# Performance work log

Hardware: AMD Instinct MI355X
Metric: run time of the kernel (lower is better)

Reference implementation:

```python
import jax, jax.numpy as jnp
import numpy as np

RMAX = 5.0   # max_radius
NB = 8       # bessel bases
NSH = 9      # (lmax+1)^2, lmax=2
S = 4        # message passing steps


def _rms(x):
    return x * jax.lax.rsqrt(jnp.mean(x * x, axis=-1, keepdims=True) + 1e-6)


def _mlp(x, w1, b1, w2, b2):
    # 2-layer MLP (base_mlp_depth=2) with silu activation + rms_norm output
    return _rms(jax.nn.silu(x @ w1 + b1) @ w2 + b2)


def _sh(u):
    # real spherical harmonics up to l=2, component normalization (e3nn style), u: [E,3] unit vectors
    x, y, z = u[:, 0], u[:, 1], u[:, 2]
    s3, s5, s15 = 3.0 ** 0.5, 5.0 ** 0.5, 15.0 ** 0.5
    return jnp.stack([
        jnp.ones_like(x),
        s3 * x, s3 * y, s3 * z,
        s15 * x * y, s15 * y * z, 0.5 * s5 * (3.0 * z * z - 1.0),
        s15 * x * z, 0.5 * s15 * (x * x - y * y)], axis=1)


def setup_inputs() -> dict:
    key = jax.random.key(0)
    ks = iter(jax.random.split(key, 64))
    N, E, D, H, L, BOND = 20000, 640000, 128, 256, 128, 16

    def w(shape, fan):
        return jax.random.normal(next(ks), shape, jnp.float32) / np.float32(np.sqrt(fan))

    return dict(
        pos=jax.random.normal(next(ks), (N, 3), jnp.float32),
        c_in=jnp.ones((1,), jnp.float32),
        atom_type_index=jax.random.randint(next(ks), (N,), 0, 20),
        atom_code_index=jax.random.randint(next(ks), (N,), 0, 10),
        residue_code_index=jax.random.randint(next(ks), (N,), 0, 25),
        residue_sequence_index=jnp.zeros((N,), jnp.int32),  # max_sequence_length=1
        senders=jax.random.randint(next(ks), (E,), 0, N),
        receivers=jax.random.randint(next(ks), (E,), 0, N),
        bond_mask=jax.random.randint(next(ks), (E,), 0, 2),
        emb_at=w((20, 32), 1.0), emb_ac=w((10, 32), 1.0),
        emb_rc=w((25, 32), 1.0), emb_ri=w((1, 32), 1.0),
        emb_bond=w((2, BOND), 1.0),
        nenc_w1=w((D, H), D), nenc_b1=jnp.zeros((H,), jnp.float32),
        nenc_w2=w((H, L), H), nenc_b2=jnp.zeros((L,), jnp.float32),
        eenc_w1=w((NB * NSH + BOND, H), NB * NSH + BOND), eenc_b1=jnp.zeros((H,), jnp.float32),
        eenc_w2=w((H, L), H), eenc_b2=jnp.zeros((L,), jnp.float32),
        msg_w1=w((S, 3 * L, H), 3 * L), msg_b1=jnp.zeros((S, H), jnp.float32),
        msg_w2=w((S, H, L), H), msg_b2=jnp.zeros((S, L), jnp.float32),
        gate_w=w((S, L, 1), L), gate_b=jnp.zeros((S, 1), jnp.float32),
        upd_w1=w((S, 2 * L, H), 2 * L), upd_b1=jnp.zeros((S, H), jnp.float32),
        upd_w2=w((S, H, L), H), upd_b2=jnp.zeros((S, L), jnp.float32),
        head_w1=w((L, H), L), head_b1=jnp.zeros((H,), jnp.float32),
        head_w2=w((H, 3), H), head_b2=jnp.zeros((3,), jnp.float32),
    )


def reference(pos, c_in, atom_type_index, atom_code_index, residue_code_index,
              residue_sequence_index, senders, receivers, bond_mask,
              emb_at, emb_ac, emb_rc, emb_ri, emb_bond,
              nenc_w1, nenc_b1, nenc_w2, nenc_b2,
              eenc_w1, eenc_b1, eenc_w2, eenc_b2,
              msg_w1, msg_b1, msg_w2, msg_b2, gate_w, gate_b,
              upd_w1, upd_b1, upd_w2, upd_b2,
              head_w1, head_b1, head_w2, head_b2):
    N = pos.shape[0]
    E = senders.shape[0]

    # --- update_features: embeddings + edge vectors ---
    node_emb = jnp.concatenate([
        emb_at[atom_type_index], emb_ac[atom_code_index],
        emb_rc[residue_code_index], emb_ri[residue_sequence_index]], axis=1)  # [N,128]
    bond_emb = emb_bond[bond_mask]                                            # [E,16]

    up = pos / c_in
    vec = up[senders] - up[receivers]                                         # [E,3]
    r = jnp.sqrt(jnp.sum(vec * vec, axis=-1) + 1e-12)                         # [E]
    u = vec / r[:, None]

    # Bessel RBF: sqrt(2/rmax) * sin(n*pi*r/rmax) / r
    n = jnp.arange(1, NB + 1, dtype=jnp.float32)
    rbf = jnp.sqrt(2.0 / RMAX) * jnp.sin(n[None, :] * jnp.pi * r[:, None] / RMAX) / r[:, None]
    # cosine distance cutoff envelope
    cut = 0.5 * (jnp.cos(jnp.pi * jnp.minimum(r, RMAX) / RMAX) + 1.0) * (r < RMAX)

    ylm = _sh(u)                                                              # [E,9]
    radial = (rbf[:, :, None] * ylm[:, None, :]).reshape(E, NB * NSH) * cut[:, None]

    # --- encoders ---
    h = _mlp(node_emb, nenc_w1, nenc_b1, nenc_w2, nenc_b2)                    # [N,L]
    e = _mlp(jnp.concatenate([radial, bond_emb], axis=1),
             eenc_w1, eenc_b1, eenc_w2, eenc_b2)                              # [E,L]

    # --- message passing: gather -> MLP -> sigmoid-gate * cutoff -> scatter ---
    for s in range(S):
        m = _mlp(jnp.concatenate([h[senders], h[receivers], e], axis=1),
                 msg_w1[s], msg_b1[s], msg_w2[s], msg_b2[s])                  # [E,L]
        g = jax.nn.sigmoid(m @ gate_w[s] + gate_b[s]) * cut[:, None]          # [E,1]
        agg = jax.ops.segment_sum(m * g, receivers, num_segments=N)           # [N,L]
        h = h + _mlp(jnp.concatenate([h, agg], axis=1),
                     upd_w1[s], upd_b1[s], upd_w2[s], upd_b2[s])
        e = e + m

    # --- head: predict per-node 3-vector ---
    return jax.nn.silu(h @ head_w1 + head_b1) @ head_w2 + head_b2             # [N,3]
```

## Files before the change

kernel.cpp:

```cpp
#include <hip/hip_runtime.h>
#include <hip/hip_bf16.h>
#include <math.h>


#define TILE   16
#define STRIDE 20

using short8 = __attribute__((ext_vector_type(8))) short;
using f32x4  = __attribute__((ext_vector_type(4))) float;

__device__ __forceinline__ float silu_f(float x) {
  return x / (1.0f + __expf(-x));
}
__device__ __forceinline__ unsigned short f2b(float x) {
  union { __hip_bfloat16 b; unsigned short u; } v;
  v.b = __float2bfloat16(x);
  return v.u;
}
__device__ __forceinline__ float b2f(unsigned short h) {
  union { unsigned u; float f; } v; v.u = ((unsigned)h) << 16;
  return v.f;
}

__global__ __launch_bounds__(256) void pack_w_kernel(
    const float* __restrict__ src, unsigned short* __restrict__ dst,
    int Kreal, int KS, int NF)
{
  const int N = NF * 16;
  const int total = NF * KS * 512;
  for (int idx = blockIdx.x * 256 + threadIdx.x; idx < total; idx += gridDim.x * 256) {
    const int nf  = idx / (KS * 512);
    const int rem = idx - nf * (KS * 512);
    const int kk  = rem >> 9;
    const int p   = rem & 511;
    const int l   = p >> 3, j = p & 7;
    const int c   = nf * 16 + (l & 15);
    const int k   = kk * 32 + ((l >> 4) << 3) + j;
    dst[idx] = (k < Kreal) ? f2b(src[(size_t)k * N + c]) : (unsigned short)0;
  }
}

template<int KS1>
__device__ __forceinline__ void mfma_l1_compute(const unsigned short* __restrict__ x1,
                                                const unsigned short* __restrict__ w1p,
                                                int tid, f32x4 acc[8])
{
  const int w  = tid >> 6;
  const int l  = tid & 63;
  const int lr = l & 15;
  const int lk = (l >> 4) << 3;
  const int RS = KS1 * 32;
  const f32x4 zz = {0.f, 0.f, 0.f, 0.f};
  #pragma unroll
  for (int i = 0; i < 8; ++i) acc[i] = zz;

  for (int kk = 0; kk < KS1; ++kk) {
    short8 af[2];
    #pragma unroll
    for (int mf = 0; mf < 2; ++mf) {
      const int r = mf * 16 + lr;
      const int k = kk * 32 + lk;
      af[mf] = *(const short8*)&x1[r * RS + ((((k >> 3) ^ (r & 7))) << 3)];
    }
    #pragma unroll
    for (int nf = 0; nf < 4; ++nf) {
      const int nfg = w * 4 + nf;
      const short8 bf = *(const short8*)&w1p[(size_t)(((nfg * KS1) + kk) * 64 + l) * 8];
      #pragma unroll
      for (int mf = 0; mf < 2; ++mf)
        acc[mf * 4 + nf] = __builtin_amdgcn_mfma_f32_16x16x32_bf16(af[mf], bf, acc[mf * 4 + nf], 0, 0, 0);
    }
  }
}

__device__ __forceinline__ void l1_store_silu(const f32x4 acc[8],
                                              const float* __restrict__ b1,
                                              unsigned short* __restrict__ hsm,
                                              int tid)
{
  const int w = tid >> 6, l = tid & 63, lr = l & 15;
  #pragma unroll
  for (int nf = 0; nf < 4; ++nf) {
    const int c = (w * 4 + nf) * 16 + lr;
    const float bias = b1[c];
    #pragma unroll
    for (int mf = 0; mf < 2; ++mf) {
      #pragma unroll
      for (int q = 0; q < 4; ++q) {
        const int r = mf * 16 + ((l >> 4) << 2) + q;
        const float v = silu_f(acc[mf * 4 + nf][q] + bias);
        hsm[r * 256 + (((c >> 3) ^ (r & 7)) << 3) + (c & 7)] = f2b(v);
      }
    }
  }
}

__device__ __forceinline__ void mfma_l2(const unsigned short* __restrict__ hsm,
                                        const unsigned short* __restrict__ w2p,
                                        const float* __restrict__ b2,
                                        int tid, f32x4 acc2[4])
{
  const int w  = tid >> 6;
  const int l  = tid & 63;
  const int lr = l & 15;
  const int lk = (l >> 4) << 3;
  const f32x4 zz = {0.f, 0.f, 0.f, 0.f};
  #pragma unroll
  for (int i = 0; i < 4; ++i) acc2[i] = zz;

  for (int kk = 0; kk < 8; ++kk) {
    short8 af[2];
    #pragma unroll
    for (int mf = 0; mf < 2; ++mf) {
      const int r = mf * 16 + lr;
      const int k = kk * 32 + lk;
      af[mf] = *(const short8*)&hsm[r * 256 + (((k >> 3) ^ (r & 7)) << 3)];
    }
    #pragma unroll
    for (int nf2 = 0; nf2 < 2; ++nf2) {
      const int nfg = w * 2 + nf2;
      const short8 bf = *(const short8*)&w2p[(size_t)(((nfg * 8) + kk) * 64 + l) * 8];
      #pragma unroll
      for (int mf = 0; mf < 2; ++mf)
        acc2[mf * 2 + nf2] = __builtin_amdgcn_mfma_f32_16x16x32_bf16(af[mf], bf, acc2[mf * 2 + nf2], 0, 0, 0);
    }
  }
  #pragma unroll
  for (int nf2 = 0; nf2 < 2; ++nf2) {
    const float bias = b2[(w * 2 + nf2) * 16 + lr];
    #pragma unroll
    for (int mf = 0; mf < 2; ++mf) {
      #pragma unroll
      for (int q = 0; q < 4; ++q) acc2[mf * 2 + nf2][q] += bias;
    }
  }
}

__device__ __forceinline__ void rms_reduce(const f32x4 acc2[4], float* rsum,
                                           int tid, float mval[2][2][4])
{
  const int l = tid & 63;
  #pragma unroll
  for (int mf = 0; mf < 2; ++mf) {
    #pragma unroll
    for (int q = 0; q < 4; ++q) {
      float s = acc2[mf * 2][q] * acc2[mf * 2][q]
              + acc2[mf * 2 + 1][q] * acc2[mf * 2 + 1][q];
      s += __shfl_xor(s, 1); s += __shfl_xor(s, 2);
      s += __shfl_xor(s, 4); s += __shfl_xor(s, 8);
      if ((l & 15) == 0)
        atomicAdd(&rsum[mf * 16 + ((l >> 4) << 2) + q], s);
    }
  }
  __syncthreads();
  #pragma unroll
  for (int mf = 0; mf < 2; ++mf) {
    #pragma unroll
    for (int q = 0; q < 4; ++q) {
      const int r = mf * 16 + ((l >> 4) << 2) + q;
      const float inv = rsqrtf(rsum[r] * (1.0f / 128.0f) + 1e-6f);
      #pragma unroll
      for (int nf2 = 0; nf2 < 2; ++nf2)
        mval[mf][nf2][q] = acc2[mf * 2 + nf2][q] * inv;
    }
  }
}

__global__ __launch_bounds__(256, 5) void edge_enc_mfma(
    const float* __restrict__ pos, const float* __restrict__ c_in,
    const int* __restrict__ snd, const int* __restrict__ rcv,
    const int* __restrict__ bnd, const float* __restrict__ embb,
    const unsigned short* __restrict__ w1p, const float* __restrict__ b1,
    const unsigned short* __restrict__ w2p, const float* __restrict__ b2,
    unsigned short* __restrict__ e_g, float* __restrict__ cutb, int E)
{
  __shared__ __align__(16) unsigned short smem[32 * 256];
  unsigned short* x1  = smem;
  unsigned short* hsm = smem;
  __shared__ float grbf[32][8];
  __shared__ float gylm[32][9];
  __shared__ float gcut[32];
  __shared__ int   gbond[32];
  __shared__ float rsum[32];
  const int tid = threadIdx.x;
  const int e0  = blockIdx.x * 32;

  if (tid < 32) {
    rsum[tid] = 0.f;
    const int ed = min(e0 + tid, E - 1);
    const int sa = snd[ed], ra = rcv[ed];
    const float ci = c_in[0];
    const float vx = (pos[sa * 3 + 0] - pos[ra * 3 + 0]) / ci;
    const float vy = (pos[sa * 3 + 1] - pos[ra * 3 + 1]) / ci;
    const float vz = (pos[sa * 3 + 2] - pos[ra * 3 + 2]) / ci;
    const float r  = sqrtf(vx * vx + vy * vy + vz * vz + 1e-12f);
    const float ir = 1.0f / r;
    const float ux = vx * ir, uy = vy * ir, uz = vz * ir;
    const float PI = 3.14159265358979323846f;
    const float pr = PI * r * 0.2f;
    const float c0 = 0.632455532033675866f;
    #pragma unroll
    for (int n = 0; n < 8; ++n)
      grbf[tid][n] = c0 * sinf((float)(n + 1) * pr) * ir;
    const float cv = 0.5f * (cosf(PI * fminf(r, 5.0f) * 0.2f) + 1.0f)
                   * (r < 5.0f ? 1.0f : 0.0f);
    gcut[tid] = cv;
    if (e0 + tid < E) cutb[e0 + tid] = cv;
    const float s3  = 1.7320508075688772f;
    const float s5  = 2.2360679774997896f;
    const float s15 = 3.8729833462074170f;
    gylm[tid][0] = 1.0f;
    gylm[tid][1] = s3 * ux; gylm[tid][2] = s3 * uy; gylm[tid][3] = s3 * uz;
    gylm[tid][4] = s15 * ux * uy; gylm[tid][5] = s15 * uy * uz;
    gylm[tid][6] = 0.5f * s5 * (3.0f * uz * uz - 1.0f);
    gylm[tid][7] = s15 * ux * uz;
    gylm[tid][8] = 0.5f * s15 * (ux * ux - uy * uy);
    gbond[tid] = bnd[ed];
  }
  __syncthreads();
  for (int i = tid; i < 32 * 16; i += 256) {
    const int r = i >> 4, g = i & 15;
    union { short8 v; unsigned short u[8]; } t;
    #pragma unroll
    for (int j = 0; j < 8; ++j) {
      const int k = g * 8 + j;
      float v;
      if (k < 72) { const int n = k / 9, mm = k - 9 * n; v = grbf[r][n] * gylm[r][mm] * gcut[r]; }
      else if (k < 88) v = embb[gbond[r] * 16 + (k - 72)];
      else v = 0.f;
      t.u[j] = f2b(v);
    }
    *(short8*)&x1[r * 128 + ((g ^ (r & 7)) << 3)] = t.v;
  }
  __syncthreads();
  f32x4 acc1[8];
  mfma_l1_compute<4>(x1, w1p, tid, acc1);
  __syncthreads();
  l1_store_silu(acc1, b1, hsm, tid);
  __syncthreads();
  f32x4 acc2[4];
  mfma_l2(hsm, w2p, b2, tid, acc2);
  float mval[2][2][4];
  rms_reduce(acc2, rsum, tid, mval);
  const int l = tid & 63, w = tid >> 6, lr = l & 15;
  #pragma unroll
  for (int mf = 0; mf < 2; ++mf) {
    #pragma unroll
    for (int q = 0; q < 4; ++q) {
      const int r = mf * 16 + ((l >> 4) << 2) + q;
      const int ed = e0 + r;
      if (ed < E) {
        #pragma unroll
        for (int nf2 = 0; nf2 < 2; ++nf2) {
          const int c2 = (w * 2 + nf2) * 16 + lr;
          e_g[(size_t)ed * 128 + c2] = f2b(mval[mf][nf2][q]);
        }
      }
    }
  }
}

__global__ __launch_bounds__(256, 5) void msg_mfma(
    const unsigned short* __restrict__ hb, unsigned short* __restrict__ e_g,
    float* __restrict__ agg, const float* __restrict__ cutb,
    const int* __restrict__ snd, const int* __restrict__ rcv,
    const unsigned short* __restrict__ w1p, const float* __restrict__ b1,
    const unsigned short* __restrict__ w2p, const float* __restrict__ b2,
    const float* __restrict__ gw, const float* __restrict__ gb, int E)
{
  __shared__ __align__(16) unsigned short smem[32 * 384];
  unsigned short* x1  = smem;
  unsigned short* hsm = smem;
  __shared__ int   snd_s[32], rcv_s[32];
  __shared__ float cut_s[32];
  __shared__ float rsum[32], gsum[32];
  const int tid = threadIdx.x;
  const int e0  = blockIdx.x * 32;

  if (tid < 32) {
    rsum[tid] = 0.f; gsum[tid] = 0.f;
    const int ed = min(e0 + tid, E - 1);
    snd_s[tid] = snd[ed]; rcv_s[tid] = rcv[ed]; cut_s[tid] = cutb[ed];
  }
  __syncthreads();
  for (int i = tid; i < 32 * 48; i += 256) {
    const int r = i / 48, g = i - r * 48;
    short8 t;
    if (g < 32) {
      const int node = (g < 16) ? snd_s[r] : rcv_s[r];
      t = *(const short8*)&hb[(size_t)node * 128 + (g & 15) * 8];
    } else {
      const int ed = min(e0 + r, E - 1);
      t = *(const short8*)&e_g[(size_t)ed * 128 + (g - 32) * 8];
    }
    *(short8*)&x1[r * 384 + ((g ^ (r & 7)) << 3)] = t;
  }
  __syncthreads();
  f32x4 acc1[8];
  mfma_l1_compute<12>(x1, w1p, tid, acc1);

  const int l = tid & 63, w = tid >> 6, lr = l & 15;
  float eold[16];
  {
    int idx = 0;
    #pragma unroll
    for (int mf = 0; mf < 2; ++mf) {
      #pragma unroll
      for (int q = 0; q < 4; ++q) {
        const int r = mf * 16 + ((l >> 4) << 2) + q;
        #pragma unroll
        for (int nf2 = 0; nf2 < 2; ++nf2) {
          const int k = 256 + (w * 2 + nf2) * 16 + lr;
          eold[idx++] = b2f(x1[r * 384 + (((k >> 3) ^ (r & 7)) << 3) + (k & 7)]);
        }
      }
    }
  }
  __syncthreads();
  l1_store_silu(acc1, b1, hsm, tid);
  __syncthreads();
  f32x4 acc2[4];
  mfma_l2(hsm, w2p, b2, tid, acc2);
  float mval[2][2][4];
  rms_reduce(acc2, rsum, tid, mval);

  const float gw0 = gw[(w * 2 + 0) * 16 + lr];
  const float gw1 = gw[(w * 2 + 1) * 16 + lr];
  #pragma unroll
  for (int mf = 0; mf < 2; ++mf) {
    #pragma unroll
    for (int q = 0; q < 4; ++q) {
      float p = mval[mf][0][q] * gw0 + mval[mf][1][q] * gw1;
      p += __shfl_xor(p, 1); p += __shfl_xor(p, 2);
      p += __shfl_xor(p, 4); p += __shfl_xor(p, 8);
      if ((l & 15) == 0)
        atomicAdd(&gsum[mf * 16 + ((l >> 4) << 2) + q], p);
    }
  }
  __syncthreads();
  const float gbv = gb[0];
  {
    int idx = 0;
    #pragma unroll
    for (int mf = 0; mf < 2; ++mf) {
      #pragma unroll
      for (int q = 0; q < 4; ++q) {
        const int r = mf * 16 + ((l >> 4) << 2) + q;
        const int ed = e0 + r;
        if (ed < E) {
          const float gr = cut_s[r] / (1.0f + __expf(-(gsum[r] + gbv)));
          const int rv = rcv_s[r];
          #pragma unroll
          for (int nf2 = 0; nf2 < 2; ++nf2) {
            const int c2 = (w * 2 + nf2) * 16 + lr;
            const float m = mval[mf][nf2][q];
            e_g[(size_t)ed * 128 + c2] = f2b(eold[idx] + m);
            atomicAdd(&agg[(size_t)rv * 128 + c2], m * gr);
            ++idx;
          }
        } else {
          idx += 2;
        }
      }
    }
  }
}

__global__ __launch_bounds__(256, 5) void upd_mfma(
    float* __restrict__ h, unsigned short* __restrict__ hb,
    float* __restrict__ agg,
    const unsigned short* __restrict__ w1p, const float* __restrict__ b1,
    const unsigned short* __restrict__ w2p, const float* __restrict__ b2,
    int N)
{
  __shared__ __align__(16) unsigned short smem[32 * 256];
  unsigned short* x1  = smem;
  unsigned short* hsm = smem;
  __shared__ float rsum[32];
  const int tid = threadIdx.x;
  const int n0  = blockIdx.x * 32;
  if (tid < 32) rsum[tid] = 0.f;
  __syncthreads();
  for (int i = tid; i < 32 * 32; i += 256) {
    const int r = i >> 5, g = i & 31;
    const int n = min(n0 + r, N - 1);
    short8 t;
    if (g < 16) {
      t = *(const short8*)&hb[(size_t)n * 128 + g * 8];
    } else {
      const float4 f0 = *(const float4*)&agg[(size_t)n * 128 + (g - 16) * 8];
      const float4 f1 = *(const float4*)&agg[(size_t)n * 128 + (g - 16) * 8 + 4];
      union { short8 v; unsigned short u[8]; } tt;
      tt.u[0] = f2b(f0.x); tt.u[1] = f2b(f0.y); tt.u[2] = f2b(f0.z); tt.u[3] = f2b(f0.w);
      tt.u[4] = f2b(f1.x); tt.u[5] = f2b(f1.y); tt.u[6] = f2b(f1.z); tt.u[7] = f2b(f1.w);
      t = tt.v;
    }
    *(short8*)&x1[r * 256 + ((g ^ (r & 7)) << 3)] = t;
  }
  __syncthreads();
  for (int i = tid; i < 1024; i += 256) {
    const int r = i >> 5, c4 = i & 31;
    const int n = n0 + r;
    if (n < N) *(float4*)&agg[(size_t)n * 128 + c4 * 4] = make_float4(0.f, 0.f, 0.f, 0.f);
  }
  f32x4 acc1[8];
  mfma_l1_compute<8>(x1, w1p, tid, acc1);
  __syncthreads();
  l1_store_silu(acc1, b1, hsm, tid);
  __syncthreads();
  f32x4 acc2[4];
  mfma_l2(hsm, w2p, b2, tid, acc2);
  float mval[2][2][4];
  rms_reduce(acc2, rsum, tid, mval);
  const int l = tid & 63, w = tid >> 6, lr = l & 15;
  #pragma unroll
  for (int mf = 0; mf < 2; ++mf) {
    #pragma unroll
    for (int q = 0; q < 4; ++q) {
      const int r = mf * 16 + ((l >> 4) << 2) + q;
      const int n = n0 + r;
      if (n < N) {
        #pragma unroll
        for (int nf2 = 0; nf2 < 2; ++nf2) {
          const int c2 = (w * 2 + nf2) * 16 + lr;
          const float nh = h[(size_t)n * 128 + c2] + mval[mf][nf2][q];
          h[(size_t)n * 128 + c2]  = nh;
          hb[(size_t)n * 128 + c2] = f2b(nh);
        }
      }
    }
  }
}


__device__ __forceinline__ float loadE(const float* p)          { return *p; }
__device__ __forceinline__ float loadE(const __hip_bfloat16* p) { return __bfloat162float(*p); }
__device__ __forceinline__ void  storeE(float* p, float v)          { *p = v; }
__device__ __forceinline__ void  storeE(__hip_bfloat16* p, float v) { *p = __float2bfloat16(v); }

template<int K1>
__device__ __forceinline__ void layer1_silu(const float* __restrict__ xs,
                                            const float* __restrict__ w1,
                                            const float* __restrict__ b1,
                                            float* __restrict__ hs, int tid)
{
  const int jh = tid & 127;
  const int tp = tid >> 7;
  const int tbase = 8 * tp;
  float a[8] = {0,0,0,0,0,0,0,0};
  float b[8] = {0,0,0,0,0,0,0,0};
  const float* wp = w1 + jh;
  for (int k = 0; k < K1; ++k) {
    const float4 x0 = *(const float4*)&xs[k*STRIDE + tbase];
    const float4 x1 = *(const float4*)&xs[k*STRIDE + tbase + 4];
    const float wa = wp[k*256];
    const float wb = wp[k*256 + 128];
    a[0] = fmaf(x0.x, wa, a[0]); a[1] = fmaf(x0.y, wa, a[1]);
    a[2] = fmaf(x0.z, wa, a[2]); a[3] = fmaf(x0.w, wa, a[3]);
    a[4] = fmaf(x1.x, wa, a[4]); a[5] = fmaf(x1.y, wa, a[5]);
    a[6] = fmaf(x1.z, wa, a[6]); a[7] = fmaf(x1.w, wa, a[7]);
    b[0] = fmaf(x0.x, wb, b[0]); b[1] = fmaf(x0.y, wb, b[1]);
    b[2] = fmaf(x0.z, wb, b[2]); b[3] = fmaf(x0.w, wb, b[3]);
    b[4] = fmaf(x1.x, wb, b[4]); b[5] = fmaf(x1.y, wb, b[5]);
    b[6] = fmaf(x1.z, wb, b[6]); b[7] = fmaf(x1.w, wb, b[7]);
  }
  const float ba = b1[jh];
  const float bb = b1[jh + 128];
  float4 oa0, oa1, ob0, ob1;
  oa0.x = silu_f(a[0] + ba); oa0.y = silu_f(a[1] + ba);
  oa0.z = silu_f(a[2] + ba); oa0.w = silu_f(a[3] + ba);
  oa1.x = silu_f(a[4] + ba); oa1.y = silu_f(a[5] + ba);
  oa1.z = silu_f(a[6] + ba); oa1.w = silu_f(a[7] + ba);
  ob0.x = silu_f(b[0] + bb); ob0.y = silu_f(b[1] + bb);
  ob0.z = silu_f(b[2] + bb); ob0.w = silu_f(b[3] + bb);
  ob1.x = silu_f(b[4] + bb); ob1.y = silu_f(b[5] + bb);
  ob1.z = silu_f(b[6] + bb); ob1.w = silu_f(b[7] + bb);
  *(float4*)&hs[jh*STRIDE + tbase]           = oa0;
  *(float4*)&hs[jh*STRIDE + tbase + 4]       = oa1;
  *(float4*)&hs[(jh+128)*STRIDE + tbase]     = ob0;
  *(float4*)&hs[(jh+128)*STRIDE + tbase + 4] = ob1;
}

__device__ __forceinline__ void layer2_bias(const float* __restrict__ hs,
                                            const float* __restrict__ w2,
                                            const float* __restrict__ b2,
                                            int tid, float cA[4], float cB[4])
{
  const int dh = tid & 63;
  const int tq = tid >> 6;
  const int tbase = 4 * tq;
  cA[0]=cA[1]=cA[2]=cA[3]=0.0f;
  cB[0]=cB[1]=cB[2]=cB[3]=0.0f;
  const float* wp = w2 + dh;
  for (int k = 0; k < 256; ++k) {
    const float4 hv = *(const float4*)&hs[k*STRIDE + tbase];
    const float wa = wp[k*128];
    const float wb = wp[k*128 + 64];
    cA[0] = fmaf(hv.x, wa, cA[0]); cA[1] = fmaf(hv.y, wa, cA[1]);
    cA[2] = fmaf(hv.z, wa, cA[2]); cA[3] = fmaf(hv.w, wa, cA[3]);
    cB[0] = fmaf(hv.x, wb, cB[0]); cB[1] = fmaf(hv.y, wb, cB[1]);
    cB[2] = fmaf(hv.z, wb, cB[2]); cB[3] = fmaf(hv.w, wb, cB[3]);
  }
  const float b2a = b2[dh];
  const float b2b = b2[dh + 64];
  #pragma unroll
  for (int tt = 0; tt < 4; ++tt) { cA[tt] += b2a; cB[tt] += b2b; }
}

__device__ __forceinline__ void rms4(float cA[4], float cB[4])
{
  float s[4];
  #pragma unroll
  for (int tt = 0; tt < 4; ++tt) s[tt] = cA[tt]*cA[tt] + cB[tt]*cB[tt];
  #pragma unroll
  for (int off = 32; off; off >>= 1) {
    #pragma unroll
    for (int tt = 0; tt < 4; ++tt) s[tt] += __shfl_xor(s[tt], off);
  }
  #pragma unroll
  for (int tt = 0; tt < 4; ++tt) {
    const float inv = rsqrtf(s[tt] * (1.0f/128.0f) + 1e-6f);
    cA[tt] *= inv; cB[tt] *= inv;
  }
}

__global__ __launch_bounds__(256) void zero_kernel(float4* __restrict__ p, int n4)
{
  const int i = blockIdx.x * 256 + threadIdx.x;
  if (i < n4) p[i] = make_float4(0.f, 0.f, 0.f, 0.f);
}

__global__ __launch_bounds__(256) void node_enc_kernel(
    const int* __restrict__ ati, const int* __restrict__ aci,
    const int* __restrict__ rci, const int* __restrict__ rsi,
    const float* __restrict__ emb_at, const float* __restrict__ emb_ac,
    const float* __restrict__ emb_rc, const float* __restrict__ emb_ri,
    const float* __restrict__ w1, const float* __restrict__ b1,
    const float* __restrict__ w2, const float* __restrict__ b2,
    float* __restrict__ h, unsigned short* __restrict__ hb, int N)
{
  __shared__ __align__(16) float xs[128*STRIDE];
  __shared__ __align__(16) float hs[256*STRIDE];
  __shared__ int idx_s[4][TILE];
  const int tid = threadIdx.x;
  const int n0 = blockIdx.x * TILE;
  if (tid < TILE) {
    const int n = min(n0 + tid, N - 1);
    idx_s[0][tid] = ati[n]; idx_s[1][tid] = aci[n];
    idx_s[2][tid] = rci[n]; idx_s[3][tid] = rsi[n];
  }
  __syncthreads();
  for (int i = tid; i < TILE*128; i += 256) {
    const int t = i >> 7, k = i & 127;
    const int seg = k >> 5, kk = k & 31;
    const float* tab = (seg == 0) ? emb_at : (seg == 1) ? emb_ac
                     : (seg == 2) ? emb_rc : emb_ri;
    xs[k*STRIDE + t] = tab[idx_s[seg][t]*32 + kk];
  }
  __syncthreads();
  layer1_silu<128>(xs, w1, b1, hs, tid);
  __syncthreads();
  float cA[4], cB[4];
  layer2_bias(hs, w2, b2, tid, cA, cB);
  rms4(cA, cB);
  const int dh = tid & 63, tq = tid >> 6;
  #pragma unroll
  for (int tt = 0; tt < 4; ++tt) {
    const int n = n0 + 4*tq + tt;
    if (n < N) {
      h[(size_t)n*128 + dh]      = cA[tt];
      h[(size_t)n*128 + dh + 64] = cB[tt];
      if (hb) {
        hb[(size_t)n*128 + dh]      = f2b(cA[tt]);
        hb[(size_t)n*128 + dh + 64] = f2b(cB[tt]);
      }
    }
  }
}

template<typename ET>
__global__ __launch_bounds__(256) void edge_enc_kernel(
    const float* __restrict__ pos, const float* __restrict__ c_in,
    const int* __restrict__ snd, const int* __restrict__ rcv,
    const int* __restrict__ bnd, const float* __restrict__ emb_bond,
    const float* __restrict__ w1, const float* __restrict__ b1,
    const float* __restrict__ w2, const float* __restrict__ b2,
    ET* __restrict__ e, float* __restrict__ cutb, int E)
{
  __shared__ __align__(16) float xs[88*STRIDE];
  __shared__ __align__(16) float hs[256*STRIDE];
  __shared__ float grbf[TILE][8];
  __shared__ float gylm[TILE][9];
  __shared__ float gcut[TILE];
  __shared__ int   gbond[TILE];
  const int tid = threadIdx.x;
  const int e0 = blockIdx.x * TILE;
  if (tid < TILE) {
    const int ed = min(e0 + tid, E - 1);
    const int sa = snd[ed], ra = rcv[ed];
    const float ci = c_in[0];
    const float vx = (pos[sa*3+0] - pos[ra*3+0]) / ci;
    const float vy = (pos[sa*3+1] - pos[ra*3+1]) / ci;
    const float vz = (pos[sa*3+2] - pos[ra*3+2]) / ci;
    const float r  = sqrtf(vx*vx + vy*vy + vz*vz + 1e-12f);
    const float ir = 1.0f / r;
    const float ux = vx*ir, uy = vy*ir, uz = vz*ir;
    const float PI = 3.14159265358979323846f;
    const float pr = PI * r * 0.2f;
    const float c0 = 0.632455532033675866f;
    #pragma unroll
    for (int n = 0; n < 8; ++n)
      grbf[tid][n] = c0 * sinf((float)(n + 1) * pr) * ir;
    const float cv = 0.5f * (cosf(PI * fminf(r, 5.0f) * 0.2f) + 1.0f)
                   * (r < 5.0f ? 1.0f : 0.0f);
    gcut[tid] = cv;
    cutb[ed] = cv;
    const float s3  = 1.7320508075688772f;
    const float s5  = 2.2360679774997896f;
    const float s15 = 3.8729833462074170f;
    gylm[tid][0] = 1.0f;
    gylm[tid][1] = s3*ux; gylm[tid][2] = s3*uy; gylm[tid][3] = s3*uz;
    gylm[tid][4] = s15*ux*uy; gylm[tid][5] = s15*uy*uz;
    gylm[tid][6] = 0.5f*s5*(3.0f*uz*uz - 1.0f);
    gylm[tid][7] = s15*ux*uz;
    gylm[tid][8] = 0.5f*s15*(ux*ux - uy*uy);
    gbond[tid] = bnd[ed];
  }
  __syncthreads();
  for (int i = tid; i < TILE*88; i += 256) {
    const int t = i & 15, k = i >> 4;
    float v;
    if (k < 72) {
      const int n = k / 9, m = k - 9*n;
      v = grbf[t][n] * gylm[t][m] * gcut[t];
    } else {
      v = emb_bond[gbond[t]*16 + (k - 72)];
    }
    xs[k*STRIDE + t] = v;
  }
  __syncthreads();
  layer1_silu<88>(xs, w1, b1, hs, tid);
  __syncthreads();
  float cA[4], cB[4];
  layer2_bias(hs, w2, b2, tid, cA, cB);
  rms4(cA, cB);
  const int dh = tid & 63, tq = tid >> 6;
  #pragma unroll
  for (int tt = 0; tt < 4; ++tt) {
    const int ed = e0 + 4*tq + tt;
    if (ed < E) {
      storeE(&e[(size_t)ed*128 + dh],      cA[tt]);
      storeE(&e[(size_t)ed*128 + dh + 64], cB[tt]);
    }
  }
}

template<typename ET>
__global__ __launch_bounds__(256) void msg_kernel(
    const float* __restrict__ h, ET* __restrict__ e,
    float* __restrict__ agg, const float* __restrict__ cutb,
    const int* __restrict__ snd, const int* __restrict__ rcv,
    const float* __restrict__ w1, const float* __restrict__ b1,
    const float* __restrict__ w2, const float* __restrict__ b2,
    const float* __restrict__ gw, const float* __restrict__ gb,
    int E)
{
  __shared__ __align__(16) float xs[384*STRIDE];
  __shared__ __align__(16) float hs[256*STRIDE];
  __shared__ int   snd_s[TILE], rcv_s[TILE];
  __shared__ float cut_s[TILE];
  const int tid = threadIdx.x;
  const int e0 = blockIdx.x * TILE;
  if (tid < TILE) {
    const int ed = min(e0 + tid, E - 1);
    snd_s[tid] = snd[ed]; rcv_s[tid] = rcv[ed]; cut_s[tid] = cutb[ed];
  }
  __syncthreads();
  for (int i = tid; i < TILE*384; i += 256) {
    const int t = i / 384, k = i - t*384;
    float v;
    if (k < 128)      v = h[(size_t)snd_s[t]*128 + k];
    else if (k < 256) v = h[(size_t)rcv_s[t]*128 + (k - 128)];
    else {
      const int ed = min(e0 + t, E - 1);
      v = loadE(&e[(size_t)ed*128 + (k - 256)]);
    }
    xs[k*STRIDE + t] = v;
  }
  __syncthreads();
  layer1_silu<384>(xs, w1, b1, hs, tid);
  __syncthreads();
  float cA[4], cB[4];
  layer2_bias(hs, w2, b2, tid, cA, cB);
  rms4(cA, cB);
  const int dh = tid & 63, tq = tid >> 6;
  const float gwa = gw[dh], gwb = gw[dh + 64];
  const float gbv = gb[0];
  float gv[4];
  #pragma unroll
  for (int tt = 0; tt < 4; ++tt) gv[tt] = cA[tt]*gwa + cB[tt]*gwb;
  #pragma unroll
  for (int off = 32; off; off >>= 1) {
    #pragma unroll
    for (int tt = 0; tt < 4; ++tt) gv[tt] += __shfl_xor(gv[tt], off);
  }
  #pragma unroll
  for (int tt = 0; tt < 4; ++tt) {
    const int t = 4*tq + tt;
    const int ed = e0 + t;
    if (ed < E) {
      const float g = cut_s[t] / (1.0f + __expf(-(gv[tt] + gbv)));
      const float eoA = xs[(256 + dh)*STRIDE + t];
      const float eoB = xs[(256 + dh + 64)*STRIDE + t];
      storeE(&e[(size_t)ed*128 + dh],      eoA + cA[tt]);
      storeE(&e[(size_t)ed*128 + dh + 64], eoB + cB[tt]);
      const int rv = rcv_s[t];
      atomicAdd(&agg[(size_t)rv*128 + dh],      cA[tt]*g);
      atomicAdd(&agg[(size_t)rv*128 + dh + 64], cB[tt]*g);
    }
  }
}

__global__ __launch_bounds__(256) void upd_kernel(
    float* __restrict__ h, const float* __restrict__ agg,
    const float* __restrict__ w1, const float* __restrict__ b1,
    const float* __restrict__ w2, const float* __restrict__ b2,
    int N)
{
  __shared__ __align__(16) float xs[256*STRIDE];
  __shared__ __align__(16) float hs[256*STRIDE];
  const int tid = threadIdx.x;
  const int n0 = blockIdx.x * TILE;
  for (int i = tid; i < TILE*256; i += 256) {
    const int t = i >> 8, k = i & 255;
    const int n = min(n0 + t, N - 1);
    const float v = (k < 128) ? h[(size_t)n*128 + k]
                              : agg[(size_t)n*128 + (k - 128)];
    xs[k*STRIDE + t] = v;
  }
  __syncthreads();
  layer1_silu<256>(xs, w1, b1, hs, tid);
  __syncthreads();
  float cA[4], cB[4];
  layer2_bias(hs, w2, b2, tid, cA, cB);
  rms4(cA, cB);
  const int dh = tid & 63, tq = tid >> 6;
  #pragma unroll
  for (int tt = 0; tt < 4; ++tt) {
    const int t = 4*tq + tt;
    const int n = n0 + t;
    if (n < N) {
      h[(size_t)n*128 + dh]      = xs[dh*STRIDE + t] + cA[tt];
      h[(size_t)n*128 + dh + 64] = xs[(dh + 64)*STRIDE + t] + cB[tt];
    }
  }
}

__global__ __launch_bounds__(256) void head_kernel(
    const float* __restrict__ h,
    const float* __restrict__ w1, const float* __restrict__ b1,
    const float* __restrict__ w2, const float* __restrict__ b2,
    float* __restrict__ out, int N)
{
  __shared__ __align__(16) float xs[128*STRIDE];
  __shared__ __align__(16) float hs[256*STRIDE];
  const int tid = threadIdx.x;
  const int n0 = blockIdx.x * TILE;
  for (int i = tid; i < TILE*128; i += 256) {
    const int t = i >> 7, k = i & 127;
    const int n = min(n0 + t, N - 1);
    xs[k*STRIDE + t] = h[(size_t)n*128 + k];
  }
  __syncthreads();
  layer1_silu<128>(xs, w1, b1, hs, tid);
  __syncthreads();
  if (tid < 48) {
    const int t = tid / 3, o = tid - 3*(tid/3);
    float acc = b2[o];
    for (int k = 0; k < 256; ++k)
      acc = fmaf(hs[k*STRIDE + t], w2[k*3 + o], acc);
    const int n = n0 + t;
    if (n < N) out[(size_t)n*3 + o] = acc;
  }
}

extern "C" void kernel_launch(void* const* d_in, const int* in_sizes, int n_in,
                              void* d_out, int out_size, void* d_ws, size_t ws_size,
                              hipStream_t stream)
{
  const float* pos      = (const float*)d_in[0];
  const float* c_in     = (const float*)d_in[1];
  const int*   ati      = (const int*)d_in[2];
  const int*   aci      = (const int*)d_in[3];
  const int*   rci      = (const int*)d_in[4];
  const int*   rsi      = (const int*)d_in[5];
  const int*   snd      = (const int*)d_in[6];
  const int*   rcv      = (const int*)d_in[7];
  const int*   bnd      = (const int*)d_in[8];
  const float* emb_at   = (const float*)d_in[9];
  const float* emb_ac   = (const float*)d_in[10];
  const float* emb_rc   = (const float*)d_in[11];
  const float* emb_ri   = (const float*)d_in[12];
  const float* emb_bond = (const float*)d_in[13];
  const float* nenc_w1  = (const float*)d_in[14];
  const float* nenc_b1  = (const float*)d_in[15];
  const float* nenc_w2  = (const float*)d_in[16];
  const float* nenc_b2  = (const float*)d_in[17];
  const float* eenc_w1  = (const float*)d_in[18];
  const float* eenc_b1  = (const float*)d_in[19];
  const float* eenc_w2  = (const float*)d_in[20];
  const float* eenc_b2  = (const float*)d_in[21];
  const float* msg_w1   = (const float*)d_in[22];
  const float* msg_b1   = (const float*)d_in[23];
  const float* msg_w2   = (const float*)d_in[24];
  const float* msg_b2   = (const float*)d_in[25];
  const float* gate_w   = (const float*)d_in[26];
  const float* gate_b   = (const float*)d_in[27];
  const float* upd_w1   = (const float*)d_in[28];
  const float* upd_b1   = (const float*)d_in[29];
  const float* upd_w2   = (const float*)d_in[30];
  const float* upd_b2   = (const float*)d_in[31];
  const float* head_w1  = (const float*)d_in[32];
  const float* head_b1  = (const float*)d_in[33];
  const float* head_w2  = (const float*)d_in[34];
  const float* head_b2  = (const float*)d_in[35];

  const int N = in_sizes[0] / 3;
  const int E = in_sizes[6];

  char* ws = (char*)d_ws;
  float* hbuf           = (float*)ws;           ws += (size_t)N * 128 * sizeof(float);
  unsigned short* hbb   = (unsigned short*)ws;  ws += (size_t)N * 128 * sizeof(unsigned short);
  float* aggbuf         = (float*)ws;           ws += (size_t)N * 128 * sizeof(float);
  float* cutbuf         = (float*)ws;           ws += (size_t)E * sizeof(float);
  unsigned short* packs = (unsigned short*)ws;
  const size_t eenc_w1p_o = 0;
  const size_t eenc_w2p_o = eenc_w1p_o + 16*4*512;
  const size_t msg_w1p_o  = eenc_w2p_o + 8*8*512;
  const size_t msg_w2p_o  = msg_w1p_o + 4*(size_t)(16*12*512);
  const size_t upd_w1p_o  = msg_w2p_o + 4*(size_t)(8*8*512);
  const size_t upd_w2p_o  = upd_w1p_o + 4*(size_t)(16*8*512);
  const size_t packs_end  = upd_w2p_o + 4*(size_t)(8*8*512);
  ws += packs_end * sizeof(unsigned short);
  unsigned short* ebuf_mfma = (unsigned short*)ws;
  const size_t need_mfma = (size_t)(ws - (char*)d_ws) + (size_t)E * 128 * sizeof(unsigned short);

  const int nb_n16 = (N + TILE - 1) / TILE;
  const int n4     = N * 128 / 4;

  if (ws_size >= need_mfma) {
    const int nb_e32 = (E + 31) / 32;
    const int nb_n32 = (N + 31) / 32;

    pack_w_kernel<<<96, 256, 0, stream>>>(eenc_w1, packs + eenc_w1p_o, 88, 4, 16);
    pack_w_kernel<<<96, 256, 0, stream>>>(eenc_w2, packs + eenc_w2p_o, 256, 8, 8);
    for (int s = 0; s < 4; ++s) {
      pack_w_kernel<<<96, 256, 0, stream>>>(msg_w1 + (size_t)s*384*256,
          packs + msg_w1p_o + (size_t)s*16*12*512, 384, 12, 16);
      pack_w_kernel<<<96, 256, 0, stream>>>(msg_w2 + (size_t)s*256*128,
          packs + msg_w2p_o + (size_t)s*8*8*512, 256, 8, 8);
      pack_w_kernel<<<96, 256, 0, stream>>>(upd_w1 + (size_t)s*256*256,
          packs + upd_w1p_o + (size_t)s*16*8*512, 256, 8, 16);
      pack_w_kernel<<<96, 256, 0, stream>>>(upd_w2 + (size_t)s*256*128,
          packs + upd_w2p_o + (size_t)s*8*8*512, 256, 8, 8);
    }

    node_enc_kernel<<<nb_n16, 256, 0, stream>>>(
        ati, aci, rci, rsi, emb_at, emb_ac, emb_rc, emb_ri,
        nenc_w1, nenc_b1, nenc_w2, nenc_b2, hbuf, hbb, N);

    edge_enc_mfma<<<nb_e32, 256, 0, stream>>>(
        pos, c_in, snd, rcv, bnd, emb_bond,
        packs + eenc_w1p_o, eenc_b1, packs + eenc_w2p_o, eenc_b2,
        ebuf_mfma, cutbuf, E);

    zero_kernel<<<(n4 + 255) / 256, 256, 0, stream>>>((float4*)aggbuf, n4);

    for (int s = 0; s < 4; ++s) {
      msg_mfma<<<nb_e32, 256, 0, stream>>>(
          hbb, ebuf_mfma, aggbuf, cutbuf, snd, rcv,
          packs + msg_w1p_o + (size_t)s*16*12*512, msg_b1 + (size_t)s*256,
          packs + msg_w2p_o + (size_t)s*8*8*512,   msg_b2 + (size_t)s*128,
          gate_w + (size_t)s*128, gate_b + s, E);
      upd_mfma<<<nb_n32, 256, 0, stream>>>(
          hbuf, hbb, aggbuf,
          packs + upd_w1p_o + (size_t)s*16*8*512, upd_b1 + (size_t)s*256,
          packs + upd_w2p_o + (size_t)s*8*8*512,  upd_b2 + (size_t)s*128, N);
    }

    head_kernel<<<nb_n16, 256, 0, stream>>>(
        hbuf, head_w1, head_b1, head_w2, head_b2, (float*)d_out, N);
  } else {
    char* ws2 = (char*)d_ws;
    float* hbuf2   = (float*)ws2;   ws2 += (size_t)N * 128 * sizeof(float);
    float* aggbuf2 = (float*)ws2;   ws2 += (size_t)N * 128 * sizeof(float);
    float* cutbuf2 = (float*)ws2;   ws2 += (size_t)E * sizeof(float);
    __hip_bfloat16* ebuf = (__hip_bfloat16*)ws2;
    const int nb_e16 = (E + TILE - 1) / TILE;

    node_enc_kernel<<<nb_n16, 256, 0, stream>>>(
        ati, aci, rci, rsi, emb_at, emb_ac, emb_rc, emb_ri,
        nenc_w1, nenc_b1, nenc_w2, nenc_b2, hbuf2, (unsigned short*)nullptr, N);

    edge_enc_kernel<__hip_bfloat16><<<nb_e16, 256, 0, stream>>>(
        pos, c_in, snd, rcv, bnd, emb_bond,
        eenc_w1, eenc_b1, eenc_w2, eenc_b2, ebuf, cutbuf2, E);

    for (int s = 0; s < 4; ++s) {
      zero_kernel<<<(n4 + 255) / 256, 256, 0, stream>>>((float4*)aggbuf2, n4);
      msg_kernel<__hip_bfloat16><<<nb_e16, 256, 0, stream>>>(
          hbuf2, ebuf, aggbuf2, cutbuf2, snd, rcv,
          msg_w1 + (size_t)s * 384 * 256, msg_b1 + (size_t)s * 256,
          msg_w2 + (size_t)s * 256 * 128, msg_b2 + (size_t)s * 128,
          gate_w + (size_t)s * 128, gate_b + s, E);
      upd_kernel<<<nb_n16, 256, 0, stream>>>(
          hbuf2, aggbuf2,
          upd_w1 + (size_t)s * 256 * 256, upd_b1 + (size_t)s * 256,
          upd_w2 + (size_t)s * 256 * 128, upd_b2 + (size_t)s * 128, N);
    }

    head_kernel<<<nb_n16, 256, 0, stream>>>(
        hbuf2, head_w1, head_b1, head_w2, head_b2, (float*)d_out, N);
  }
}
```

Baseline: 2.437 ms.

## Enlarge msg_mfma edge tile to 64 rows and move agg zeroing to separate kernel

The message kernel now handles 64 edges per block instead of 32, with inline MFMA loops where each wave computes 4 row fragments and reuses every weight fragment across them. This halves global weight-fragment loads per edge, and occupancy hints drop from 5 to 3 blocks per CU to allow the larger register and LDS footprint. The old edge features are re-read from global memory at store time instead of being held in registers. Zeroing of the aggregation buffer moves out of the update kernel into a zero_kernel launch before each step, which adds a launch and an extra pass over the buffer.

```diff
diff --git a/kernel.cpp b/kernel.cpp
--- a/kernel.cpp
+++ b/kernel.cpp
@@ -260,7 +260,7 @@
   }
 }
 
-__global__ __launch_bounds__(256, 5) void msg_mfma(
+__global__ __launch_bounds__(256, 3) void msg_mfma(
     const unsigned short* __restrict__ hb, unsigned short* __restrict__ e_g,
     float* __restrict__ agg, const float* __restrict__ cutb,
     const int* __restrict__ snd, const int* __restrict__ rcv,
@@ -268,22 +268,22 @@
     const unsigned short* __restrict__ w2p, const float* __restrict__ b2,
     const float* __restrict__ gw, const float* __restrict__ gb, int E)
 {
-  __shared__ __align__(16) unsigned short smem[32 * 384];
+  __shared__ __align__(16) unsigned short smem[64 * 384];
   unsigned short* x1  = smem;
   unsigned short* hsm = smem;
-  __shared__ int   snd_s[32], rcv_s[32];
-  __shared__ float cut_s[32];
-  __shared__ float rsum[32], gsum[32];
+  __shared__ int   snd_s[64], rcv_s[64];
+  __shared__ float cut_s[64];
+  __shared__ float rsum[64], gsum[64];
   const int tid = threadIdx.x;
-  const int e0  = blockIdx.x * 32;
-
-  if (tid < 32) {
+  const int e0  = blockIdx.x * 64;
+
+  if (tid < 64) {
     rsum[tid] = 0.f; gsum[tid] = 0.f;
     const int ed = min(e0 + tid, E - 1);
     snd_s[tid] = snd[ed]; rcv_s[tid] = rcv[ed]; cut_s[tid] = cutb[ed];
   }
   __syncthreads();
-  for (int i = tid; i < 32 * 48; i += 256) {
+  for (int i = tid; i < 64 * 48; i += 256) {
     const int r = i / 48, g = i - r * 48;
     short8 t;
     if (g < 32) {
@@ -296,38 +296,110 @@
     *(short8*)&x1[r * 384 + ((g ^ (r & 7)) << 3)] = t;
   }
   __syncthreads();
-  f32x4 acc1[8];
-  mfma_l1_compute<12>(x1, w1p, tid, acc1);
-
-  const int l = tid & 63, w = tid >> 6, lr = l & 15;
-  float eold[16];
+
+  const int w  = tid >> 6;
+  const int l  = tid & 63;
+  const int lr = l & 15;
+  const int lk = (l >> 4) << 3;
+
+  f32x4 acc1[16];
   {
-    int idx = 0;
-    #pragma unroll
-    for (int mf = 0; mf < 2; ++mf) {
+    const f32x4 zz = {0.f, 0.f, 0.f, 0.f};
+    #pragma unroll
+    for (int i = 0; i < 16; ++i) acc1[i] = zz;
+  }
+  for (int kk = 0; kk < 12; ++kk) {
+    short8 af[4];
+    #pragma unroll
+    for (int mf = 0; mf < 4; ++mf) {
+      const int r = mf * 16 + lr;
+      const int k = kk * 32 + lk;
+      af[mf] = *(const short8*)&x1[r * 384 + (((k >> 3) ^ (r & 7)) << 3)];
+    }
+    #pragma unroll
+    for (int nf = 0; nf < 4; ++nf) {
+      const short8 bf = *(const short8*)&w1p[(size_t)((((w * 4 + nf) * 12) + kk) * 64 + l) * 8];
+      #pragma unroll
+      for (int mf = 0; mf < 4; ++mf)
+        acc1[mf * 4 + nf] = __builtin_amdgcn_mfma_f32_16x16x32_bf16(af[mf], bf, acc1[mf * 4 + nf], 0, 0, 0);
+    }
+  }
+  __syncthreads();
+  #pragma unroll
+  for (int nf = 0; nf < 4; ++nf) {
+    const int c = (w * 4 + nf) * 16 + lr;
+    const float bias = b1[c];
+    #pragma unroll
+    for (int mf = 0; mf < 4; ++mf) {
       #pragma unroll
       for (int q = 0; q < 4; ++q) {
         const int r = mf * 16 + ((l >> 4) << 2) + q;
-        #pragma unroll
-        for (int nf2 = 0; nf2 < 2; ++nf2) {
-          const int k = 256 + (w * 2 + nf2) * 16 + lr;
-          eold[idx++] = b2f(x1[r * 384 + (((k >> 3) ^ (r & 7)) << 3) + (k & 7)]);
-        }
+        const float v = silu_f(acc1[mf * 4 + nf][q] + bias);
+        hsm[r * 256 + (((c >> 3) ^ (r & 7)) << 3) + (c & 7)] = f2b(v);
       }
     }
   }
   __syncthreads();
-  l1_store_silu(acc1, b1, hsm, tid);
-  __syncthreads();
-  f32x4 acc2[4];
-  mfma_l2(hsm, w2p, b2, tid, acc2);
-  float mval[2][2][4];
-  rms_reduce(acc2, rsum, tid, mval);
-
+  f32x4 acc2[8];
+  {
+    const f32x4 zz = {0.f, 0.f, 0.f, 0.f};
+    #pragma unroll
+    for (int i = 0; i < 8; ++i) acc2[i] = zz;
+  }
+  for (int kk = 0; kk < 8; ++kk) {
+    short8 af[4];
+    #pragma unroll
+    for (int mf = 0; mf < 4; ++mf) {
+      const int r = mf * 16 + lr;
+      const int k = kk * 32 + lk;
+      af[mf] = *(const short8*)&hsm[r * 256 + (((k >> 3) ^ (r & 7)) << 3)];
+    }
+    #pragma unroll
+    for (int nf2 = 0; nf2 < 2; ++nf2) {
+      const short8 bf = *(const short8*)&w2p[(size_t)((((w * 2 + nf2) * 8) + kk) * 64 + l) * 8];
+      #pragma unroll
+      for (int mf = 0; mf < 4; ++mf)
+        acc2[mf * 2 + nf2] = __builtin_amdgcn_mfma_f32_16x16x32_bf16(af[mf], bf, acc2[mf * 2 + nf2], 0, 0, 0);
+    }
+  }
+  #pragma unroll
+  for (int nf2 = 0; nf2 < 2; ++nf2) {
+    const float bias = b2[(w * 2 + nf2) * 16 + lr];
+    #pragma unroll
+    for (int mf = 0; mf < 4; ++mf) {
+      #pragma unroll
+      for (int q = 0; q < 4; ++q) acc2[mf * 2 + nf2][q] += bias;
+    }
+  }
+  float mval[4][2][4];
+  #pragma unroll
+  for (int mf = 0; mf < 4; ++mf) {
+    #pragma unroll
+    for (int q = 0; q < 4; ++q) {
+      float s = acc2[mf * 2][q] * acc2[mf * 2][q]
+              + acc2[mf * 2 + 1][q] * acc2[mf * 2 + 1][q];
+      s += __shfl_xor(s, 1); s += __shfl_xor(s, 2);
+      s += __shfl_xor(s, 4); s += __shfl_xor(s, 8);
+      if ((l & 15) == 0)
+        atomicAdd(&rsum[mf * 16 + ((l >> 4) << 2) + q], s);
+    }
+  }
+  __syncthreads();
+  #pragma unroll
+  for (int mf = 0; mf < 4; ++mf) {
+    #pragma unroll
+    for (int q = 0; q < 4; ++q) {
+      const int r = mf * 16 + ((l >> 4) << 2) + q;
+      const float inv = rsqrtf(rsum[r] * (1.0f / 128.0f) + 1e-6f);
+      #pragma unroll
+      for (int nf2 = 0; nf2 < 2; ++nf2)
+        mval[mf][nf2][q] = acc2[mf * 2 + nf2][q] * inv;
+    }
+  }
   const float gw0 = gw[(w * 2 + 0) * 16 + lr];
   const float gw1 = gw[(w * 2 + 1) * 16 + lr];
   #pragma unroll
-  for (int mf = 0; mf < 2; ++mf) {
+  for (int mf = 0; mf < 4; ++mf) {
     #pragma unroll
     for (int q = 0; q < 4; ++q) {
       float p = mval[mf][0][q] * gw0 + mval[mf][1][q] * gw1;
@@ -339,27 +411,22 @@
   }
   __syncthreads();
   const float gbv = gb[0];
-  {
-    int idx = 0;
-    #pragma unroll
-    for (int mf = 0; mf < 2; ++mf) {
-      #pragma unroll
-      for (int q = 0; q < 4; ++q) {
-        const int r = mf * 16 + ((l >> 4) << 2) + q;
-        const int ed = e0 + r;
-        if (ed < E) {
-          const float gr = cut_s[r] / (1.0f + __expf(-(gsum[r] + gbv)));
-          const int rv = rcv_s[r];
-          #pragma unroll
-          for (int nf2 = 0; nf2 < 2; ++nf2) {
-            const int c2 = (w * 2 + nf2) * 16 + lr;
-            const float m = mval[mf][nf2][q];
-            e_g[(size_t)ed * 128 + c2] = f2b(eold[idx] + m);
-            atomicAdd(&agg[(size_t)rv * 128 + c2], m * gr);
-            ++idx;
-          }
-        } else {
-          idx += 2;
+  #pragma unroll
+  for (int mf = 0; mf < 4; ++mf) {
+    #pragma unroll
+    for (int q = 0; q < 4; ++q) {
+      const int r = mf * 16 + ((l >> 4) << 2) + q;
+      const int ed = e0 + r;
+      if (ed < E) {
+        const float gr = cut_s[r] / (1.0f + __expf(-(gsum[r] + gbv)));
+        const int rv = rcv_s[r];
+        #pragma unroll
+        for (int nf2 = 0; nf2 < 2; ++nf2) {
+          const int c2 = (w * 2 + nf2) * 16 + lr;
+          const float m = mval[mf][nf2][q];
+          const float eo = b2f(e_g[(size_t)ed * 128 + c2]);
+          e_g[(size_t)ed * 128 + c2] = f2b(eo + m);
+          atomicAdd(&agg[(size_t)rv * 128 + c2], m * gr);
         }
       }
     }
@@ -368,7 +435,7 @@
 
 __global__ __launch_bounds__(256, 5) void upd_mfma(
     float* __restrict__ h, unsigned short* __restrict__ hb,
-    float* __restrict__ agg,
+    const float* __restrict__ agg,
     const unsigned short* __restrict__ w1p, const float* __restrict__ b1,
     const unsigned short* __restrict__ w2p, const float* __restrict__ b2,
     int N)
@@ -398,11 +465,6 @@
     *(short8*)&x1[r * 256 + ((g ^ (r & 7)) << 3)] = t;
   }
   __syncthreads();
-  for (int i = tid; i < 1024; i += 256) {
-    const int r = i >> 5, c4 = i & 31;
-    const int n = n0 + r;
-    if (n < N) *(float4*)&agg[(size_t)n * 128 + c4 * 4] = make_float4(0.f, 0.f, 0.f, 0.f);
-  }
   f32x4 acc1[8];
   mfma_l1_compute<8>(x1, w1p, tid, acc1);
   __syncthreads();
@@ -850,6 +912,7 @@
 
   if (ws_size >= need_mfma) {
     const int nb_e32 = (E + 31) / 32;
+    const int nb_e64 = (E + 63) / 64;
     const int nb_n32 = (N + 31) / 32;
 
     pack_w_kernel<<<96, 256, 0, stream>>>(eenc_w1, packs + eenc_w1p_o, 88, 4, 16);
@@ -874,10 +937,9 @@
         packs + eenc_w1p_o, eenc_b1, packs + eenc_w2p_o, eenc_b2,
         ebuf_mfma, cutbuf, E);
 
-    zero_kernel<<<(n4 + 255) / 256, 256, 0, stream>>>((float4*)aggbuf, n4);
-
     for (int s = 0; s < 4; ++s) {
-      msg_mfma<<<nb_e32, 256, 0, stream>>>(
+      zero_kernel<<<(n4 + 255) / 256, 256, 0, stream>>>((float4*)aggbuf, n4);
+      msg_mfma<<<nb_e64, 256, 0, stream>>>(
           hbb, ebuf_mfma, aggbuf, cutbuf, snd, rcv,
           packs + msg_w1p_o + (size_t)s*16*12*512, msg_b1 + (size_t)s*256,
           packs + msg_w2p_o + (size_t)s*8*8*512,   msg_b2 + (size_t)s*128,
```

Result: slower. 3.121 ms (+28.1%).
